# Kernel tuning notes

Measured on AMD Instinct MI355X. Metric: run time of the kernel, lower is better.

Reference implementation:

```python
import jax, jax.numpy as jnp
import numpy as np

B, S, EMBED, DK, DV, M = 8, 1024, 1024, 512, 512, 64


def setup_inputs() -> dict:
    key = jax.random.key(0)
    ks = jax.random.split(key, 9)
    query_in = jax.random.normal(ks[0], (B, S, EMBED), dtype=jnp.float32)
    key_in = jax.random.normal(ks[1], (B, S, EMBED), dtype=jnp.float32)
    value_in = jax.random.normal(ks[2], (B, S, EMBED), dtype=jnp.float32)
    lim = 1.0 / np.sqrt(EMBED)  # nn.Linear default init range
    u = lambda k, shape: jax.random.uniform(k, shape, minval=-lim, maxval=lim, dtype=jnp.float32)
    return {
        'query_in': query_in, 'key_in': key_in, 'value_in': value_in,
        'Wq': u(ks[3], (DK, EMBED)), 'bq': u(ks[4], (DK,)),
        'Wk': u(ks[5], (DK, EMBED)), 'bk': u(ks[6], (DK,)),
        'Wv': u(ks[7], (DV, EMBED)), 'bv': u(ks[8], (DV,)),
    }


def _select_landmarks(k_proj, m):
    # Original code runs recursive RLS sampling (random, host-side) over the m
    # segment-rows of key.reshape(B, m, seg, d) and gathers m of them back,
    # then flattens to (B, S, d). We use a deterministic data-dependent
    # selection (rows ranked by squared norm) with identical gather structure.
    Bb, Ss, d = k_proj.shape
    seg = Ss // m
    kr = k_proj.reshape(Bb, m, seg, d)
    scores = jnp.sum(kr * kr, axis=(2, 3))                      # [B, m]
    idx = jnp.argsort(-scores, axis=1)                          # [B, m]
    land = jnp.take_along_axis(kr, idx[:, :, None, None], axis=1)
    return land.reshape(Bb, Ss, d)                              # [B, S, d]


def reference(query_in, key_in, value_in, Wq, bq, Wk, bk, Wv, bv):
    scaling = DK ** -0.25  # 1/sqrt(sqrt(d_k)), applied to both q and k
    q = (jnp.einsum('bse,de->bsd', query_in, Wq) + bq) * scaling
    k = (jnp.einsum('bse,de->bsd', key_in, Wk) + bk) * scaling
    v = jnp.einsum('bse,de->bsd', value_in, Wv) + bv

    kl = _select_landmarks(k, M)                                # [B, S, DK]
    # is_decoder_self_attn is hard-coded True upstream -> q_landmarks = q,
    # so kernel_2 == kernel_1.
    kernel_1 = jax.nn.softmax(jnp.einsum('bqd,bkd->bqk', q, kl), axis=-1)
    kernel_2 = kernel_1
    kernel_3 = jax.nn.softmax(jnp.einsum('bqd,bkd->bqk', q, k), axis=-1)

    k2_inv = jnp.linalg.pinv(kernel_2)                          # [B, S, S] batched SVD
    out = jnp.einsum('bqk,bkd->bqd', jnp.einsum('bqm,bmk->bqk', kernel_1, k2_inv),
                     jnp.einsum('bqk,bkd->bqd', kernel_3, v))
    # dropout is identity in eval mode
    return out
```

## Files before the change

kernel.cpp:

```cpp
#include <hip/hip_runtime.h>
#include <hip/hip_bf16.h>

#define SS   1024
#define DKK  512

typedef __hip_bfloat16 bf16;
typedef __attribute__((ext_vector_type(8))) short s16x8;
typedef __attribute__((ext_vector_type(8))) unsigned short u16x8;
typedef __attribute__((ext_vector_type(4))) float f32x4;

#define WS_W(z)  ((48ull << 20) + ((size_t)(z) << 20))
#define WS_Q     (52ull << 20)
#define WS_K     (60ull << 20)
#define WS_VT    (68ull << 20)
#define WS_LG    (0ull)

__device__ __forceinline__ void async_ld16(const void* g, void* s) {
  __builtin_amdgcn_global_load_lds(
      (const __attribute__((address_space(1))) void*)g,
      (__attribute__((address_space(3))) void*)s, 16, 0, 0);
}

__device__ __forceinline__ unsigned short f2bfu(float f) {
  return __builtin_bit_cast(unsigned short, __float2bfloat16(f));
}
__device__ __forceinline__ float bfu2f(unsigned short u) {
  unsigned int i = ((unsigned int)u) << 16;
  return __builtin_bit_cast(float, i);
}

__global__ __launch_bounds__(256)
void convert_w(const float* __restrict__ w0, const float* __restrict__ w1,
               const float* __restrict__ w2, char* __restrict__ ws)
{
  const int bx = blockIdx.x;
  const int z = bx >> 8, local = bx & 255;
  const float* src = (z == 0) ? w0 : (z == 1) ? w1 : w2;
  unsigned short* dst = (unsigned short*)(ws + WS_W(z));
  const int i = local * 2048 + threadIdx.x * 8;
  const float4* s = (const float4*)(src + i);
  float4 a = s[0], b = s[1];
  ushort4 o0, o1;
  o0.x = f2bfu(a.x); o0.y = f2bfu(a.y); o0.z = f2bfu(a.z); o0.w = f2bfu(a.w);
  o1.x = f2bfu(b.x); o1.y = f2bfu(b.y); o1.z = f2bfu(b.z); o1.w = f2bfu(b.w);
  ((ushort4*)(dst + i))[0] = o0;
  ((ushort4*)(dst + i))[1] = o1;
}

template<int BM, int K, int LDA, int LDB>
__device__ __forceinline__ void gemm_core(const bf16* __restrict__ A,
                                          const bf16* __restrict__ Bw,
                                          int bm, int bn,
                                          short* As, short* Bs, f32x4* acc)
{
  constexpr int MI = BM / 32;
  constexpr int AR = BM / 4;
  const int tid  = threadIdx.x;
  const int lane = tid & 63;
  const int wave = tid >> 6;
  const int l8   = lane >> 3;
  const int kch  = ((lane & 7) ^ l8) * 8;
  const bf16* ag = A  + (size_t)(bm * BM + wave * AR + l8) * LDA + kch;
  const bf16* bg = Bw + (size_t)(bn * 128 + wave * 32 + l8) * LDB + kch;
  short* AsW = As + wave * AR * 64;
  short* BsW = Bs + wave * 32 * 64;
  const int waveM = wave >> 1, waveN = wave & 1;
  const int l16  = lane & 15;
  const int quad = lane >> 4;
  const int xr   = l16 & 7;

  #pragma unroll
  for (int t = 0; t < MI * 4; ++t)
    #pragma unroll
    for (int r = 0; r < 4; ++r) acc[t][r] = 0.0f;

  for (int kt = 0; kt < K / 64; ++kt) {
    #pragma unroll
    for (int j = 0; j < AR / 8; ++j) async_ld16(ag + (size_t)j * 8 * LDA, AsW + j * 8 * 64);
    #pragma unroll
    for (int j = 0; j < 4; ++j)      async_ld16(bg + (size_t)j * 8 * LDB, BsW + j * 8 * 64);
    ag += 64; bg += 64;
    __syncthreads();
    #pragma unroll
    for (int ks = 0; ks < 2; ++ks) {
      s16x8 af[MI], bfv[4];
      #pragma unroll
      for (int mi = 0; mi < MI; ++mi) {
        const int row  = waveM * (BM / 2) + mi * 16 + l16;
        const int slot = (ks * 4 + quad) ^ xr;
        af[mi] = *(const s16x8*)&As[row * 64 + slot * 8];
      }
      #pragma unroll
      for (int ni = 0; ni < 4; ++ni) {
        const int row  = waveN * 64 + ni * 16 + l16;
        const int slot = (ks * 4 + quad) ^ xr;
        bfv[ni] = *(const s16x8*)&Bs[row * 64 + slot * 8];
      }
      #pragma unroll
      for (int mi = 0; mi < MI; ++mi)
        #pragma unroll
        for (int ni = 0; ni < 4; ++ni)
          acc[mi * 4 + ni] = __builtin_amdgcn_mfma_f32_16x16x32_bf16(
              af[mi], bfv[ni], acc[mi * 4 + ni], 0, 0, 0);
    }
    __syncthreads();
  }
}

template<int K, int LDA, int LDB>
__device__ __forceinline__ void gemm_core_f32a(const float* __restrict__ A,
                                               const bf16* __restrict__ Bw,
                                               int bm, int bn,
                                               short* As, short* Bs, f32x4* acc)
{
  const int tid  = threadIdx.x;
  const int lane = tid & 63;
  const int wave = tid >> 6;
  const int l8   = lane >> 3;
  const int kch  = ((lane & 7) ^ l8) * 8;
  const bf16* bg = Bw + (size_t)(bn * 256 + wave * 64 + l8) * LDB + kch;
  short* BsW = Bs + wave * 64 * 64;
  const int arow = tid >> 3;
  const int ag8  = tid & 7;
  const int slotA = (ag8 ^ (arow & 7)) * 8;
  const float* ag = A + (size_t)(bm * 128 + arow) * LDA + ag8 * 8;
  const int waveM = wave >> 1, waveN = wave & 1;
  const int l16  = lane & 15;
  const int quad = lane >> 4;
  const int xr   = l16 & 7;

  #pragma unroll
  for (int t = 0; t < 32; ++t)
    #pragma unroll
    for (int r = 0; r < 4; ++r) acc[t][r] = 0.0f;

  for (int kt = 0; kt < K / 64; ++kt) {
    #pragma unroll
    for (int j = 0; j < 8; ++j) async_ld16(bg + (size_t)j * 8 * LDB, BsW + j * 8 * 64);
    bg += 64;
    #pragma unroll
    for (int p = 0; p < 4; ++p) {
      const float4* s = (const float4*)(ag + (size_t)p * 32 * LDA);
      float4 a = s[0], b = s[1];
      u16x8 v;
      v[0] = f2bfu(a.x); v[1] = f2bfu(a.y); v[2] = f2bfu(a.z); v[3] = f2bfu(a.w);
      v[4] = f2bfu(b.x); v[5] = f2bfu(b.y); v[6] = f2bfu(b.z); v[7] = f2bfu(b.w);
      *(u16x8*)&As[(p * 32 + arow) * 64 + slotA] = v;
    }
    ag += 64;
    __syncthreads();
    #pragma unroll
    for (int ks = 0; ks < 2; ++ks) {
      s16x8 af[4], bfv[8];
      #pragma unroll
      for (int mi = 0; mi < 4; ++mi) {
        const int row  = waveM * 64 + mi * 16 + l16;
        const int slot = (ks * 4 + quad) ^ xr;
        af[mi] = *(const s16x8*)&As[row * 64 + slot * 8];
      }
      #pragma unroll
      for (int ni = 0; ni < 8; ++ni) {
        const int row  = waveN * 128 + ni * 16 + l16;
        const int slot = (ks * 4 + quad) ^ xr;
        bfv[ni] = *(const s16x8*)&Bs[row * 64 + slot * 8];
      }
      #pragma unroll
      for (int mi = 0; mi < 4; ++mi)
        #pragma unroll
        for (int ni = 0; ni < 8; ++ni)
          acc[mi * 8 + ni] = __builtin_amdgcn_mfma_f32_16x16x32_bf16(
              af[mi], bfv[ni], acc[mi * 8 + ni], 0, 0, 0);
    }
    __syncthreads();
  }
}

__global__ __launch_bounds__(256, 2)
void proj_kernel(const float* __restrict__ Xq, const float* __restrict__ Xk,
                 const float* __restrict__ Xv, const bf16* __restrict__ W0,
                 const float* __restrict__ bq, const float* __restrict__ bk,
                 const float* __restrict__ bv,
                 bf16* __restrict__ qo, bf16* __restrict__ ko,
                 bf16* __restrict__ vT, float qscale)
{
  __shared__ __align__(16) short As[128 * 64];
  __shared__ __align__(16) short Bs[256 * 64];
  const int id   = blockIdx.x;
  const int xcd  = id & 7;
  const int s    = id >> 3;
  const int bn   = s & 1;
  const int pair = (s >> 1) * 8 + xcd;
  const int bm   = pair & 63;
  const int z    = pair >> 6;
  const float* A  = (z == 0) ? Xq : (z == 1) ? Xk : Xv;
  const bf16*  Bw = W0 + ((size_t)z << 19);
  const float* bias = (z == 0) ? bq : (z == 1) ? bk : bv;
  f32x4 acc[32];
  gemm_core_f32a<1024, 1024, 1024>(A, Bw, bm, bn, As, Bs, acc);

  const int lane = threadIdx.x & 63;
  const int wave = threadIdx.x >> 6;
  const int waveM = wave >> 1, waveN = wave & 1;
  const int l16 = lane & 15, quad = lane >> 4;
  const int row0 = bm * 128 + waveM * 64;
  const int col0 = bn * 256 + waveN * 128;
  const float sc = (z == 0) ? qscale : 1.0f;
  bf16* C = (z == 0) ? qo : ko;
  #pragma unroll
  for (int ni = 0; ni < 8; ++ni) {
    const int col = col0 + ni * 16 + l16;
    const float bb = bias[col];
    #pragma unroll
    for (int mi = 0; mi < 4; ++mi)
      #pragma unroll
      for (int r = 0; r < 4; ++r) {
        const int row = row0 + mi * 16 + quad * 4 + r;
        const float v = acc[mi * 8 + ni][r] + bb;
        if (z == 2)
          vT[((size_t)(row >> 10) * DKK + col) * SS + (row & (SS - 1))] =
              __float2bfloat16(v);
        else
          C[(size_t)row * DKK + col] = __float2bfloat16(v * sc);
      }
  }
}

__global__ __launch_bounds__(256, 4)
void scores_kernel(const bf16* __restrict__ q, const bf16* __restrict__ k,
                   bf16* __restrict__ lgB)
{
  __shared__ __align__(16) short As[64 * 64];
  __shared__ __align__(16) short Bs[128 * 64];
  const int z = blockIdx.z;
  const int bn = blockIdx.x, bm = blockIdx.y;
  f32x4 acc[8];
  gemm_core<64, 512, 512, 512>(q + (size_t)z * SS * DKK, k + (size_t)z * SS * DKK,
                               bm, bn, As, Bs, acc);

  const int lane = threadIdx.x & 63;
  const int wave = threadIdx.x >> 6;
  const int waveM = wave >> 1, waveN = wave & 1;
  const int l16 = lane & 15, quad = lane >> 4;
  const int row0 = bm * 64 + waveM * 32;
  const int col0 = bn * 128 + waveN * 64;
  bf16* C = lgB + (size_t)z * SS * SS;
  #pragma unroll
  for (int ni = 0; ni < 4; ++ni) {
    const int col = col0 + ni * 16 + l16;
    #pragma unroll
    for (int mi = 0; mi < 2; ++mi)
      #pragma unroll
      for (int r = 0; r < 4; ++r) {
        const int row = row0 + mi * 16 + quad * 4 + r;
        C[(size_t)row * SS + col] = __float2bfloat16(acc[mi * 4 + ni][r]);
      }
  }
}

__global__ __launch_bounds__(256)
void softmax_kernel(unsigned short* __restrict__ Pm)
{
  const int lane = threadIdx.x & 63;
  const int wv   = threadIdx.x >> 6;
  const size_t row = (size_t)blockIdx.x * 4 + wv;
  ushort4* ptr = (ushort4*)(Pm + row * SS);
  ushort4 u[4];
  float x[16];
  #pragma unroll
  for (int i = 0; i < 4; ++i) u[i] = ptr[lane + i * 64];
  #pragma unroll
  for (int i = 0; i < 4; ++i) {
    x[i * 4 + 0] = bfu2f(u[i].x); x[i * 4 + 1] = bfu2f(u[i].y);
    x[i * 4 + 2] = bfu2f(u[i].z); x[i * 4 + 3] = bfu2f(u[i].w);
  }
  float m = x[0];
  #pragma unroll
  for (int i = 1; i < 16; ++i) m = fmaxf(m, x[i]);
  #pragma unroll
  for (int off = 32; off > 0; off >>= 1) m = fmaxf(m, __shfl_xor(m, off));
  float s = 0.f;
  #pragma unroll
  for (int i = 0; i < 16; ++i) { x[i] = __expf(x[i] - m); s += x[i]; }
  #pragma unroll
  for (int off = 32; off > 0; off >>= 1) s += __shfl_xor(s, off);
  const float rs = 1.0f / s;
  #pragma unroll
  for (int i = 0; i < 4; ++i) {
    ushort4 o;
    o.x = f2bfu(x[i * 4 + 0] * rs); o.y = f2bfu(x[i * 4 + 1] * rs);
    o.z = f2bfu(x[i * 4 + 2] * rs); o.w = f2bfu(x[i * 4 + 3] * rs);
    ptr[lane + i * 64] = o;
  }
}

__global__ __launch_bounds__(256, 4)
void pv_kernel(const bf16* __restrict__ P, const bf16* __restrict__ vT,
               float* __restrict__ out)
{
  __shared__ __align__(16) short As[64 * 64];
  __shared__ __align__(16) short Bs[128 * 64];
  const int z = blockIdx.z;
  const int bn = blockIdx.x, bm = blockIdx.y;
  f32x4 acc[8];
  gemm_core<64, 1024, 1024, 1024>(P + (size_t)z * SS * SS, vT + (size_t)z * DKK * SS,
                                  bm, bn, As, Bs, acc);

  const int lane = threadIdx.x & 63;
  const int wave = threadIdx.x >> 6;
  const int waveM = wave >> 1, waveN = wave & 1;
  const int l16 = lane & 15, quad = lane >> 4;
  const int row0 = bm * 64 + waveM * 32;
  const int col0 = bn * 128 + waveN * 64;
  float* C = out + (size_t)z * SS * DKK;
  #pragma unroll
  for (int ni = 0; ni < 4; ++ni) {
    const int col = col0 + ni * 16 + l16;
    #pragma unroll
    for (int mi = 0; mi < 2; ++mi)
      #pragma unroll
      for (int r = 0; r < 4; ++r) {
        const int row = row0 + mi * 16 + quad * 4 + r;
        C[(size_t)row * DKK + col] = acc[mi * 4 + ni][r];
      }
  }
}

extern "C" void kernel_launch(void* const* d_in, const int* in_sizes, int n_in,
                              void* d_out, int out_size, void* d_ws, size_t ws_size,
                              hipStream_t stream)
{
  char* ws = (char*)d_ws;
  bf16* W0  = (bf16*)(ws + WS_W(0));
  bf16* q   = (bf16*)(ws + WS_Q);
  bf16* kk  = (bf16*)(ws + WS_K);
  bf16* vT  = (bf16*)(ws + WS_VT);
  bf16* lgB = (bf16*)(ws + WS_LG);

  const float qscale = 0.044194173824159216f;

  dim3 blk(256, 1, 1);
  hipLaunchKernelGGL(convert_w, dim3(768), blk, 0, stream,
                     (const float*)d_in[3], (const float*)d_in[5],
                     (const float*)d_in[7], ws);
  hipLaunchKernelGGL(proj_kernel, dim3(384, 1, 1), blk, 0, stream,
                     (const float*)d_in[0], (const float*)d_in[1],
                     (const float*)d_in[2], W0,
                     (const float*)d_in[4], (const float*)d_in[6],
                     (const float*)d_in[8], q, kk, vT, qscale);
  hipLaunchKernelGGL(scores_kernel, dim3(8, 16, 8), blk, 0, stream, q, kk, lgB);
  hipLaunchKernelGGL(softmax_kernel, dim3(2048, 1, 1), blk, 0, stream,
                     (unsigned short*)lgB);
  hipLaunchKernelGGL(pv_kernel, dim3(4, 16, 8), blk, 0, stream,
                     lgB, vT, (float*)d_out);
}
```

Measured before the change: 224.9 us.

## Fuse softmax into scores epilogue and PV prologue; shrink projection tile

```diff
diff --git a/kernel.cpp b/kernel.cpp
--- a/kernel.cpp
+++ b/kernel.cpp
@@ -10,6 +10,7 @@
 typedef __attribute__((ext_vector_type(4))) float f32x4;
 
 #define WS_W(z)  ((48ull << 20) + ((size_t)(z) << 20))
+#define WS_ST    (51ull << 20)
 #define WS_Q     (52ull << 20)
 #define WS_K     (60ull << 20)
 #define WS_VT    (68ull << 20)
@@ -123,14 +124,14 @@
   const int arow = tid >> 3;
   const int ag8  = tid & 7;
   const int slotA = (ag8 ^ (arow & 7)) * 8;
-  const float* ag = A + (size_t)(bm * 128 + arow) * LDA + ag8 * 8;
+  const float* ag = A + (size_t)(bm * 64 + arow) * LDA + ag8 * 8;
   const int waveM = wave >> 1, waveN = wave & 1;
   const int l16  = lane & 15;
   const int quad = lane >> 4;
   const int xr   = l16 & 7;
 
   #pragma unroll
-  for (int t = 0; t < 32; ++t)
+  for (int t = 0; t < 16; ++t)
     #pragma unroll
     for (int r = 0; r < 4; ++r) acc[t][r] = 0.0f;
 
@@ -139,7 +140,7 @@
     for (int j = 0; j < 8; ++j) async_ld16(bg + (size_t)j * 8 * LDB, BsW + j * 8 * 64);
     bg += 64;
     #pragma unroll
-    for (int p = 0; p < 4; ++p) {
+    for (int p = 0; p < 2; ++p) {
       const float4* s = (const float4*)(ag + (size_t)p * 32 * LDA);
       float4 a = s[0], b = s[1];
       u16x8 v;
@@ -151,10 +152,10 @@
     __syncthreads();
     #pragma unroll
     for (int ks = 0; ks < 2; ++ks) {
-      s16x8 af[4], bfv[8];
-      #pragma unroll
-      for (int mi = 0; mi < 4; ++mi) {
-        const int row  = waveM * 64 + mi * 16 + l16;
+      s16x8 af[2], bfv[8];
+      #pragma unroll
+      for (int mi = 0; mi < 2; ++mi) {
+        const int row  = waveM * 32 + mi * 16 + l16;
         const int slot = (ks * 4 + quad) ^ xr;
         af[mi] = *(const s16x8*)&As[row * 64 + slot * 8];
       }
@@ -165,7 +166,7 @@
         bfv[ni] = *(const s16x8*)&Bs[row * 64 + slot * 8];
       }
       #pragma unroll
-      for (int mi = 0; mi < 4; ++mi)
+      for (int mi = 0; mi < 2; ++mi)
         #pragma unroll
         for (int ni = 0; ni < 8; ++ni)
           acc[mi * 8 + ni] = __builtin_amdgcn_mfma_f32_16x16x32_bf16(
@@ -175,7 +176,7 @@
   }
 }
 
-__global__ __launch_bounds__(256, 2)
+__global__ __launch_bounds__(256, 3)
 void proj_kernel(const float* __restrict__ Xq, const float* __restrict__ Xk,
                  const float* __restrict__ Xv, const bf16* __restrict__ W0,
                  const float* __restrict__ bq, const float* __restrict__ bk,
@@ -183,26 +184,26 @@
                  bf16* __restrict__ qo, bf16* __restrict__ ko,
                  bf16* __restrict__ vT, float qscale)
 {
-  __shared__ __align__(16) short As[128 * 64];
+  __shared__ __align__(16) short As[64 * 64];
   __shared__ __align__(16) short Bs[256 * 64];
   const int id   = blockIdx.x;
   const int xcd  = id & 7;
   const int s    = id >> 3;
   const int bn   = s & 1;
   const int pair = (s >> 1) * 8 + xcd;
-  const int bm   = pair & 63;
-  const int z    = pair >> 6;
+  const int bm   = pair & 127;
+  const int z    = pair >> 7;
   const float* A  = (z == 0) ? Xq : (z == 1) ? Xk : Xv;
   const bf16*  Bw = W0 + ((size_t)z << 19);
   const float* bias = (z == 0) ? bq : (z == 1) ? bk : bv;
-  f32x4 acc[32];
+  f32x4 acc[16];
   gemm_core_f32a<1024, 1024, 1024>(A, Bw, bm, bn, As, Bs, acc);
 
   const int lane = threadIdx.x & 63;
   const int wave = threadIdx.x >> 6;
   const int waveM = wave >> 1, waveN = wave & 1;
   const int l16 = lane & 15, quad = lane >> 4;
-  const int row0 = bm * 128 + waveM * 64;
+  const int row0 = bm * 64 + waveM * 32;
   const int col0 = bn * 256 + waveN * 128;
   const float sc = (z == 0) ? qscale : 1.0f;
   bf16* C = (z == 0) ? qo : ko;
@@ -211,7 +212,7 @@
     const int col = col0 + ni * 16 + l16;
     const float bb = bias[col];
     #pragma unroll
-    for (int mi = 0; mi < 4; ++mi)
+    for (int mi = 0; mi < 2; ++mi)
       #pragma unroll
       for (int r = 0; r < 4; ++r) {
         const int row = row0 + mi * 16 + quad * 4 + r;
@@ -227,7 +228,7 @@
 
 __global__ __launch_bounds__(256, 4)
 void scores_kernel(const bf16* __restrict__ q, const bf16* __restrict__ k,
-                   bf16* __restrict__ lgB)
+                   bf16* __restrict__ lgB, float* __restrict__ stats)
 {
   __shared__ __align__(16) short As[64 * 64];
   __shared__ __align__(16) short Bs[128 * 64];
@@ -255,58 +256,137 @@
         C[(size_t)row * SS + col] = __float2bfloat16(acc[mi * 4 + ni][r]);
       }
   }
-}
-
-__global__ __launch_bounds__(256)
-void softmax_kernel(unsigned short* __restrict__ Pm)
-{
-  const int lane = threadIdx.x & 63;
-  const int wv   = threadIdx.x >> 6;
-  const size_t row = (size_t)blockIdx.x * 4 + wv;
-  ushort4* ptr = (ushort4*)(Pm + row * SS);
-  ushort4 u[4];
-  float x[16];
-  #pragma unroll
-  for (int i = 0; i < 4; ++i) u[i] = ptr[lane + i * 64];
-  #pragma unroll
-  for (int i = 0; i < 4; ++i) {
-    x[i * 4 + 0] = bfu2f(u[i].x); x[i * 4 + 1] = bfu2f(u[i].y);
-    x[i * 4 + 2] = bfu2f(u[i].z); x[i * 4 + 3] = bfu2f(u[i].w);
-  }
-  float m = x[0];
-  #pragma unroll
-  for (int i = 1; i < 16; ++i) m = fmaxf(m, x[i]);
-  #pragma unroll
-  for (int off = 32; off > 0; off >>= 1) m = fmaxf(m, __shfl_xor(m, off));
-  float s = 0.f;
-  #pragma unroll
-  for (int i = 0; i < 16; ++i) { x[i] = __expf(x[i] - m); s += x[i]; }
-  #pragma unroll
-  for (int off = 32; off > 0; off >>= 1) s += __shfl_xor(s, off);
-  const float rs = 1.0f / s;
-  #pragma unroll
-  for (int i = 0; i < 4; ++i) {
-    ushort4 o;
-    o.x = f2bfu(x[i * 4 + 0] * rs); o.y = f2bfu(x[i * 4 + 1] * rs);
-    o.z = f2bfu(x[i * 4 + 2] * rs); o.w = f2bfu(x[i * 4 + 3] * rs);
-    ptr[lane + i * 64] = o;
+  const int chunk = bn * 2 + waveN;
+  #pragma unroll
+  for (int mi = 0; mi < 2; ++mi)
+    #pragma unroll
+    for (int r = 0; r < 4; ++r) {
+      float xr4[4];
+      float m = -1e30f;
+      #pragma unroll
+      for (int ni = 0; ni < 4; ++ni) {
+        xr4[ni] = bfu2f(f2bfu(acc[mi * 4 + ni][r]));
+        m = fmaxf(m, xr4[ni]);
+      }
+      #pragma unroll
+      for (int msk = 1; msk < 16; msk <<= 1) m = fmaxf(m, __shfl_xor(m, msk));
+      float e = 0.f;
+      #pragma unroll
+      for (int ni = 0; ni < 4; ++ni) e += __expf(xr4[ni] - m);
+      #pragma unroll
+      for (int msk = 1; msk < 16; msk <<= 1) e += __shfl_xor(e, msk);
+      if (l16 == 0) {
+        const int row = row0 + mi * 16 + quad * 4 + r;
+        float2 mr; mr.x = m; mr.y = e;
+        *(float2*)&stats[(((size_t)z * SS + row) * 16 + chunk) * 2] = mr;
+      }
+    }
+}
+
+__device__ __forceinline__ void gemm_core_pv(const unsigned short* __restrict__ lg,
+                                             const bf16* __restrict__ vT,
+                                             int bm, int bn,
+                                             const float* Ml, const float* Rl,
+                                             short* As, short* Bs, f32x4* acc)
+{
+  const int tid  = threadIdx.x;
+  const int lane = tid & 63;
+  const int wave = tid >> 6;
+  const int l8   = lane >> 3;
+  const int kch  = ((lane & 7) ^ l8) * 8;
+  const bf16* bg = vT + (size_t)(bn * 128 + wave * 32 + l8) * 1024 + kch;
+  short* BsW = Bs + wave * 32 * 64;
+  const int arow = tid >> 3;
+  const int ag8  = tid & 7;
+  const int slotA = (ag8 ^ (arow & 7)) * 8;
+  const unsigned short* ag = lg + (size_t)(bm * 64 + arow) * 1024 + ag8 * 8;
+  const int waveM = wave >> 1, waveN = wave & 1;
+  const int l16  = lane & 15;
+  const int quad = lane >> 4;
+  const int xr   = l16 & 7;
+
+  #pragma unroll
+  for (int t = 0; t < 8; ++t)
+    #pragma unroll
+    for (int r = 0; r < 4; ++r) acc[t][r] = 0.0f;
+
+  for (int kt = 0; kt < 16; ++kt) {
+    #pragma unroll
+    for (int j = 0; j < 4; ++j) async_ld16(bg + (size_t)j * 8 * 1024, BsW + j * 8 * 64);
+    bg += 64;
+    #pragma unroll
+    for (int p = 0; p < 2; ++p) {
+      const int rl = p * 32 + arow;
+      u16x8 u = *(const u16x8*)(ag + (size_t)p * 32 * 1024);
+      const float M = Ml[rl], R = Rl[rl];
+      u16x8 v;
+      #pragma unroll
+      for (int j = 0; j < 8; ++j)
+        v[j] = f2bfu(__expf(bfu2f((unsigned short)u[j]) - M) * R);
+      *(u16x8*)&As[rl * 64 + slotA] = v;
+    }
+    ag += 64;
+    __syncthreads();
+    #pragma unroll
+    for (int ks = 0; ks < 2; ++ks) {
+      s16x8 af[2], bfv[4];
+      #pragma unroll
+      for (int mi = 0; mi < 2; ++mi) {
+        const int row  = waveM * 32 + mi * 16 + l16;
+        const int slot = (ks * 4 + quad) ^ xr;
+        af[mi] = *(const s16x8*)&As[row * 64 + slot * 8];
+      }
+      #pragma unroll
+      for (int ni = 0; ni < 4; ++ni) {
+        const int row  = waveN * 64 + ni * 16 + l16;
+        const int slot = (ks * 4 + quad) ^ xr;
+        bfv[ni] = *(const s16x8*)&Bs[row * 64 + slot * 8];
+      }
+      #pragma unroll
+      for (int mi = 0; mi < 2; ++mi)
+        #pragma unroll
+        for (int ni = 0; ni < 4; ++ni)
+          acc[mi * 4 + ni] = __builtin_amdgcn_mfma_f32_16x16x32_bf16(
+              af[mi], bfv[ni], acc[mi * 4 + ni], 0, 0, 0);
+    }
+    __syncthreads();
   }
 }
 
 __global__ __launch_bounds__(256, 4)
-void pv_kernel(const bf16* __restrict__ P, const bf16* __restrict__ vT,
-               float* __restrict__ out)
+void pv_kernel(const unsigned short* __restrict__ lgB, const bf16* __restrict__ vT,
+               const float* __restrict__ stats, float* __restrict__ out)
 {
   __shared__ __align__(16) short As[64 * 64];
   __shared__ __align__(16) short Bs[128 * 64];
+  __shared__ float Ml[64], Rl[64];
   const int z = blockIdx.z;
   const int bn = blockIdx.x, bm = blockIdx.y;
+  const int tid = threadIdx.x;
+
+  if (tid < 64) {
+    const int row = bm * 64 + tid;
+    const float* st = stats + ((size_t)z * SS + row) * 32;
+    float mc[16], lc[16];
+    float M = -1e30f;
+    #pragma unroll
+    for (int c = 0; c < 16; ++c) {
+      mc[c] = st[c * 2]; lc[c] = st[c * 2 + 1];
+      M = fmaxf(M, mc[c]);
+    }
+    float L = 0.f;
+    #pragma unroll
+    for (int c = 0; c < 16; ++c) L += __expf(mc[c] - M) * lc[c];
+    Ml[tid] = M; Rl[tid] = 1.0f / L;
+  }
+  __syncthreads();
+
   f32x4 acc[8];
-  gemm_core<64, 1024, 1024, 1024>(P + (size_t)z * SS * SS, vT + (size_t)z * DKK * SS,
-                                  bm, bn, As, Bs, acc);
-
-  const int lane = threadIdx.x & 63;
-  const int wave = threadIdx.x >> 6;
+  gemm_core_pv(lgB + (size_t)z * SS * SS, vT + (size_t)z * DKK * SS,
+               bm, bn, Ml, Rl, As, Bs, acc);
+
+  const int lane = tid & 63;
+  const int wave = tid >> 6;
   const int waveM = wave >> 1, waveN = wave & 1;
   const int l16 = lane & 15, quad = lane >> 4;
   const int row0 = bm * 64 + waveM * 32;
@@ -330,11 +410,12 @@
                               hipStream_t stream)
 {
   char* ws = (char*)d_ws;
-  bf16* W0  = (bf16*)(ws + WS_W(0));
-  bf16* q   = (bf16*)(ws + WS_Q);
-  bf16* kk  = (bf16*)(ws + WS_K);
-  bf16* vT  = (bf16*)(ws + WS_VT);
-  bf16* lgB = (bf16*)(ws + WS_LG);
+  bf16*  W0   = (bf16*)(ws + WS_W(0));
+  float* stat = (float*)(ws + WS_ST);
+  bf16*  q    = (bf16*)(ws + WS_Q);
+  bf16*  kk   = (bf16*)(ws + WS_K);
+  bf16*  vT   = (bf16*)(ws + WS_VT);
+  bf16*  lgB  = (bf16*)(ws + WS_LG);
 
   const float qscale = 0.044194173824159216f;
 
@@ -342,14 +423,13 @@
   hipLaunchKernelGGL(convert_w, dim3(768), blk, 0, stream,
                      (const float*)d_in[3], (const float*)d_in[5],
                      (const float*)d_in[7], ws);
-  hipLaunchKernelGGL(proj_kernel, dim3(384, 1, 1), blk, 0, stream,
+  hipLaunchKernelGGL(proj_kernel, dim3(768, 1, 1), blk, 0, stream,
                      (const float*)d_in[0], (const float*)d_in[1],
                      (const float*)d_in[2], W0,
                      (const float*)d_in[4], (const float*)d_in[6],
                      (const float*)d_in[8], q, kk, vT, qscale);
-  hipLaunchKernelGGL(scores_kernel, dim3(8, 16, 8), blk, 0, stream, q, kk, lgB);
-  hipLaunchKernelGGL(softmax_kernel, dim3(2048, 1, 1), blk, 0, stream,
-                     (unsigned short*)lgB);
+  hipLaunchKernelGGL(scores_kernel, dim3(8, 16, 8), blk, 0, stream,
+                     q, kk, lgB, stat);
   hipLaunchKernelGGL(pv_kernel, dim3(4, 16, 8), blk, 0, stream,
-                     lgB, vT, (float*)d_out);
-}
+                     (const unsigned short*)lgB, vT, stat, (float*)d_out);
+}
```

Result: no change. 220.7 us (-1.9%).
